# Kernel tuning notes

Measured on AMD Instinct MI355X. Metric: run time of the kernel, lower is better.

Reference implementation:

```python
import jax, jax.numpy as jnp
import numpy as np

N_NODES = 100000
N_EDGES = 600000
IN_FEAT = 128
OUT_FEAT = 128
NUM_RELS = 8
NUM_BASES = 4


def setup_inputs() -> dict:
    key = jax.random.key(0)
    ks = jax.random.split(key, 8)
    h = jax.random.normal(ks[0], (N_NODES, IN_FEAT), dtype=jnp.float32)
    # xavier-ish scale for params
    weight = jax.random.normal(ks[1], (NUM_BASES, IN_FEAT, OUT_FEAT), dtype=jnp.float32) * (1.0 / np.sqrt(IN_FEAT))
    w_comp = jax.random.normal(ks[2], (NUM_RELS, NUM_BASES), dtype=jnp.float32) * (1.0 / np.sqrt(NUM_BASES))
    root_weight = jax.random.normal(ks[3], (IN_FEAT, OUT_FEAT), dtype=jnp.float32) * (1.0 / np.sqrt(IN_FEAT))
    bias = jnp.zeros((OUT_FEAT,), dtype=jnp.float32)
    src = jax.random.randint(ks[4], (N_EDGES,), 0, N_NODES, dtype=jnp.int32)
    dst = jax.random.randint(ks[5], (N_EDGES,), 0, N_NODES, dtype=jnp.int32)
    rel_type = jax.random.randint(ks[6], (N_EDGES,), 0, NUM_RELS, dtype=jnp.int32)
    return {"h": h, "weight": weight, "w_comp": w_comp, "root_weight": root_weight,
            "bias": bias, "src": src, "dst": dst, "rel_type": rel_type}


def reference(h, weight, w_comp, root_weight, bias, src, dst, rel_type):
    # Basis decomposition: W[r] = sum_b w_comp[r,b] * weight[b]
    B, I, O = weight.shape
    R = w_comp.shape[0]
    W = (w_comp @ weight.reshape(B, I * O)).reshape(R, I, O)  # [R, in, out]
    # msg_e = h[src_e] @ W[rel_e]; computed as all-relation projection + gather
    # (avoids materializing [E, in, out] per-edge weights)
    proj = jnp.einsum('ni,rio->nro', h, W)          # [N, R, out]
    msg = proj[src, rel_type]                        # [E, out]
    agg = jax.ops.segment_sum(msg, dst, num_segments=h.shape[0])  # scatter-sum
    out = h @ root_weight + agg + bias
    return jax.nn.relu(out)
```

## Files before the change

kernel.cpp:

```cpp
#include <hip/hip_runtime.h>
#include <hip/hip_bf16.h>

#define N_NODES 100000
#define N_EDGES 600000
#define FEAT 128
#define NUM_RELS 8
#define NUM_BASES 4
#define NBE 2344

#define PREP_CAST 6250
#define PREP_BLDB 320
#define PREP_ZERO 392
#define PREP_GRID (PREP_CAST + PREP_BLDB + PREP_ZERO)

#define SCAN_TILES 98

typedef short bf16x8 __attribute__((ext_vector_type(8)));
typedef float f32x4  __attribute__((ext_vector_type(4)));
typedef float f32x2  __attribute__((ext_vector_type(2)));

__device__ inline short f2bf(float x) {
    __hip_bfloat16 b = __float2bfloat16(x);
    return *reinterpret_cast<short*>(&b);
}


__global__ __launch_bounds__(256) void k_prep(const float* __restrict__ h,
                                              const float* __restrict__ weight,
                                              const float* __restrict__ rw,
                                              short* __restrict__ hb,
                                              short* __restrict__ Btf,
                                              int* __restrict__ cnt,
                                              int* __restrict__ status) {
    int b = blockIdx.x;
    if (b < PREP_CAST) {
        int i = b * 256 + threadIdx.x;
        const float4* h4 = (const float4*)h;
        float4 v0 = h4[2 * i], v1 = h4[2 * i + 1];
        union { short s[8]; bf16x8 v; } u;
        u.s[0] = f2bf(v0.x); u.s[1] = f2bf(v0.y); u.s[2] = f2bf(v0.z); u.s[3] = f2bf(v0.w);
        u.s[4] = f2bf(v1.x); u.s[5] = f2bf(v1.y); u.s[6] = f2bf(v1.z); u.s[7] = f2bf(v1.w);
        ((bf16x8*)hb)[i] = u.v;
    } else if (b < PREP_CAST + PREP_BLDB) {
        int idx = (b - PREP_CAST) * 256 + threadIdx.x;
        int kc = idx >> 14;
        int e  = idx & 16383;
        int o  = e >> 7, ip = e & 127;
        float v = (kc == 0) ? rw[ip * FEAT + o]
                            : weight[(kc - 1) * FEAT * FEAT + ip * FEAT + o];
        int nt = o & 7, n16 = o >> 3;
        int ks = ip >> 5, quad = (ip >> 3) & 3, j = ip & 7;
        int lane = quad * 16 + n16;
        Btf[((kc * 4 + ks) * 8 + nt) * 512 + lane * 8 + j] = f2bf(v);
    } else {
        int i = (b - PREP_CAST - PREP_BLDB) * 256 + threadIdx.x;
        if (i < N_NODES) cnt[i] = 0;
        else if (i - N_NODES < 128) status[i - N_NODES] = 0;
    }
}

__global__ __launch_bounds__(256) void k_hist_dst(const int* __restrict__ dst,
                                                  int* __restrict__ cnt) {
    int i = blockIdx.x * 256 + threadIdx.x;
    if (i < N_EDGES) atomicAdd(&cnt[dst[i]], 1);
}

__global__ __launch_bounds__(256) void k_scan_lb(const int* __restrict__ cnt,
                                                 int* __restrict__ offs,
                                                 int* __restrict__ cursor,
                                                 int* __restrict__ status) {
    __shared__ int wsum[4];
    __shared__ int bcast;
    int bid = blockIdx.x;
    int lane = threadIdx.x & 63, wid = threadIdx.x >> 6;
    const int N4 = N_NODES / 4;
    int i4 = bid * 256 + threadIdx.x;

    const int4* cnt4 = (const int4*)cnt;
    int4 v = (i4 < N4) ? cnt4[i4] : make_int4(0, 0, 0, 0);
    int s = v.x + v.y + v.z + v.w;
    int incl = s;
#pragma unroll
    for (int d = 1; d < 64; d <<= 1) {
        int t = __shfl_up(incl, d);
        if (lane >= d) incl += t;
    }
    if (lane == 63) wsum[wid] = incl;
    __syncthreads();
    int total = wsum[0] + wsum[1] + wsum[2] + wsum[3];

    if (threadIdx.x < 64) {
        int excl = 0;
        if (bid > 0) {
            if (lane == 0)
                __hip_atomic_store(&status[bid], (total << 2) | 1,
                                   __ATOMIC_RELEASE, __HIP_MEMORY_SCOPE_AGENT);
            int winEnd = bid;
            for (;;) {
                int idx = winEnd - 64 + lane;
                int st = 2;
                if (idx >= 0) {
                    st = __hip_atomic_load(&status[idx],
                                           __ATOMIC_ACQUIRE, __HIP_MEMORY_SCOPE_AGENT);
                    while ((st & 3) == 0) {
                        __builtin_amdgcn_s_sleep(1);
                        st = __hip_atomic_load(&status[idx],
                                               __ATOMIC_ACQUIRE, __HIP_MEMORY_SCOPE_AGENT);
                    }
                }
                unsigned long long done = __ballot((st & 3) == 2);
                int contrib;
                if (done) {
                    int L = 63 - __builtin_clzll(done);
                    contrib = (lane >= L) ? (st >> 2) : 0;
                } else {
                    contrib = st >> 2;
                }
#pragma unroll
                for (int m = 1; m < 64; m <<= 1) contrib += __shfl_xor(contrib, m);
                excl += contrib;
                if (done) break;
                winEnd -= 64;
            }
        }
        if (lane == 0) {
            __hip_atomic_store(&status[bid], ((excl + total) << 2) | 2,
                               __ATOMIC_RELEASE, __HIP_MEMORY_SCOPE_AGENT);
            bcast = excl;
            if (bid == SCAN_TILES - 1) offs[N_NODES] = excl + total;
        }
    }
    __syncthreads();
    int wexcl = 0;
#pragma unroll
    for (int w = 0; w < 4; ++w) if (w < wid) wexcl += wsum[w];
    int base = bcast + wexcl + incl - s;
    if (i4 < N4) {
        int4 ex;
        ex.x = base;
        ex.y = base + v.x;
        ex.z = base + v.x + v.y;
        ex.w = base + v.x + v.y + v.z;
        ((int4*)offs)[i4]   = ex;
        ((int4*)cursor)[i4] = ex;
    }
}

__global__ __launch_bounds__(256) void k_scatter_sorted(const int* __restrict__ src,
                                                        const int* __restrict__ dst,
                                                        const int* __restrict__ rel,
                                                        int* __restrict__ cursor,
                                                        int* __restrict__ packed) {
    int e = blockIdx.x * 256 + threadIdx.x;
    if (e < N_EDGES) {
        int p = atomicAdd(&cursor[dst[e]], 1);
        packed[p] = (src[e] << 3) | rel[e];
    }
}

#define RL(pk, j) __builtin_amdgcn_readlane(pk, j)
#define EDGE_ACC(zz, c, v)                                               \
    {   f32x2 hh; hh.x = __int_as_float((v) << 16);                      \
        hh.y = __int_as_float((v) & 0xffff0000u);                        \
        f32x2 cc;                                                        \
        cc = c.x; zz[0] += cc * hh;                                      \
        cc = c.y; zz[1] += cc * hh;                                      \
        cc = c.z; zz[2] += cc * hh;                                      \
        cc = c.w; zz[3] += cc * hh; }

__global__ __launch_bounds__(256) void k_edge_z(const int* __restrict__ offs,
                                                const int* __restrict__ packed,
                                                const float* __restrict__ wc,
                                                const short* __restrict__ hb,
                                                unsigned int* __restrict__ z_u32) {
    int wid = threadIdx.x >> 6, lane = threadIdx.x & 63;
    int d0 = blockIdx.x * 8 + wid * 2;
    int s0 = offs[d0], sM = offs[d0 + 1], e1 = offs[d0 + 2];

    const float4* wc4 = (const float4*)wc;
    const unsigned int* hbu = (const unsigned int*)hb;

    f32x2 za[4] = {(f32x2)0.f, (f32x2)0.f, (f32x2)0.f, (f32x2)0.f};
    f32x2 zb[4] = {(f32x2)0.f, (f32x2)0.f, (f32x2)0.f, (f32x2)0.f};

    int baseA = s0, baseB = sM;
    while (baseA < sM || baseB < e1) {
        int mA = sM - baseA; mA = mA < 0 ? 0 : (mA > 64 ? 64 : mA);
        int mB = e1 - baseB; mB = mB < 0 ? 0 : (mB > 64 ? 64 : mB);
        int pkA = (lane < mA) ? packed[baseA + lane] : 0;
        int pkB = (lane < mB) ? packed[baseB + lane] : 0;
        int jA = 0, jB = 0;

        while (jA + 3 < mA && jB + 3 < mB) {
            int a0 = RL(pkA, jA), a1 = RL(pkA, jA + 1), a2 = RL(pkA, jA + 2), a3 = RL(pkA, jA + 3);
            int b0 = RL(pkB, jB), b1 = RL(pkB, jB + 1), b2 = RL(pkB, jB + 2), b3 = RL(pkB, jB + 3);
            unsigned int va0 = hbu[(size_t)(a0 >> 3) * 64 + lane];
            unsigned int va1 = hbu[(size_t)(a1 >> 3) * 64 + lane];
            unsigned int va2 = hbu[(size_t)(a2 >> 3) * 64 + lane];
            unsigned int va3 = hbu[(size_t)(a3 >> 3) * 64 + lane];
            unsigned int vb0 = hbu[(size_t)(b0 >> 3) * 64 + lane];
            unsigned int vb1 = hbu[(size_t)(b1 >> 3) * 64 + lane];
            unsigned int vb2 = hbu[(size_t)(b2 >> 3) * 64 + lane];
            unsigned int vb3 = hbu[(size_t)(b3 >> 3) * 64 + lane];
            float4 ca0 = wc4[a0 & 7], ca1 = wc4[a1 & 7], ca2 = wc4[a2 & 7], ca3 = wc4[a3 & 7];
            float4 cb0 = wc4[b0 & 7], cb1 = wc4[b1 & 7], cb2 = wc4[b2 & 7], cb3 = wc4[b3 & 7];
            EDGE_ACC(za, ca0, va0); EDGE_ACC(za, ca1, va1);
            EDGE_ACC(za, ca2, va2); EDGE_ACC(za, ca3, va3);
            EDGE_ACC(zb, cb0, vb0); EDGE_ACC(zb, cb1, vb1);
            EDGE_ACC(zb, cb2, vb2); EDGE_ACC(zb, cb3, vb3);
            jA += 4; jB += 4;
        }
        while (jA < mA && jB < mB) {
            int a0 = RL(pkA, jA), b0 = RL(pkB, jB);
            unsigned int va0 = hbu[(size_t)(a0 >> 3) * 64 + lane];
            unsigned int vb0 = hbu[(size_t)(b0 >> 3) * 64 + lane];
            float4 ca0 = wc4[a0 & 7], cb0 = wc4[b0 & 7];
            EDGE_ACC(za, ca0, va0);
            EDGE_ACC(zb, cb0, vb0);
            ++jA; ++jB;
        }
        while (jA + 3 < mA) {
            int a0 = RL(pkA, jA), a1 = RL(pkA, jA + 1), a2 = RL(pkA, jA + 2), a3 = RL(pkA, jA + 3);
            unsigned int va0 = hbu[(size_t)(a0 >> 3) * 64 + lane];
            unsigned int va1 = hbu[(size_t)(a1 >> 3) * 64 + lane];
            unsigned int va2 = hbu[(size_t)(a2 >> 3) * 64 + lane];
            unsigned int va3 = hbu[(size_t)(a3 >> 3) * 64 + lane];
            float4 ca0 = wc4[a0 & 7], ca1 = wc4[a1 & 7], ca2 = wc4[a2 & 7], ca3 = wc4[a3 & 7];
            EDGE_ACC(za, ca0, va0); EDGE_ACC(za, ca1, va1);
            EDGE_ACC(za, ca2, va2); EDGE_ACC(za, ca3, va3);
            jA += 4;
        }
        while (jA < mA) {
            int a0 = RL(pkA, jA);
            unsigned int va0 = hbu[(size_t)(a0 >> 3) * 64 + lane];
            float4 ca0 = wc4[a0 & 7];
            EDGE_ACC(za, ca0, va0);
            ++jA;
        }
        while (jB + 3 < mB) {
            int b0 = RL(pkB, jB), b1 = RL(pkB, jB + 1), b2 = RL(pkB, jB + 2), b3 = RL(pkB, jB + 3);
            unsigned int vb0 = hbu[(size_t)(b0 >> 3) * 64 + lane];
            unsigned int vb1 = hbu[(size_t)(b1 >> 3) * 64 + lane];
            unsigned int vb2 = hbu[(size_t)(b2 >> 3) * 64 + lane];
            unsigned int vb3 = hbu[(size_t)(b3 >> 3) * 64 + lane];
            float4 cb0 = wc4[b0 & 7], cb1 = wc4[b1 & 7], cb2 = wc4[b2 & 7], cb3 = wc4[b3 & 7];
            EDGE_ACC(zb, cb0, vb0); EDGE_ACC(zb, cb1, vb1);
            EDGE_ACC(zb, cb2, vb2); EDGE_ACC(zb, cb3, vb3);
            jB += 4;
        }
        while (jB < mB) {
            int b0 = RL(pkB, jB);
            unsigned int vb0 = hbu[(size_t)(b0 >> 3) * 64 + lane];
            float4 cb0 = wc4[b0 & 7];
            EDGE_ACC(zb, cb0, vb0);
            ++jB;
        }
        baseA += 64; baseB += 64;
    }

    unsigned int* row0 = z_u32 + (size_t)d0 * 256;
    unsigned int* row1 = row0 + 256;
#pragma unroll
    for (int b = 0; b < 4; ++b) {
        unsigned int lo0 = ((unsigned int)(unsigned short)f2bf(za[b].x));
        unsigned int hi0 = ((unsigned int)(unsigned short)f2bf(za[b].y)) << 16;
        row0[b * 64 + lane] = lo0 | hi0;
        unsigned int lo1 = ((unsigned int)(unsigned short)f2bf(zb[b].x));
        unsigned int hi1 = ((unsigned int)(unsigned short)f2bf(zb[b].y)) << 16;
        row1[b * 64 + lane] = lo1 | hi1;
    }
}

__global__ __launch_bounds__(256) void k_gemm_fused(const short* __restrict__ hb,
                                                    const short* __restrict__ z,
                                                    const short* __restrict__ Btf,
                                                    const float* __restrict__ bias,
                                                    float* __restrict__ out) {
    __shared__ short lds[FEAT * FEAT];
    int wave = threadIdx.x >> 6, lane = threadIdx.x & 63;
    int quad = lane >> 4, n16 = lane & 15;
    int base = blockIdx.x * 64 + wave * 16;

    int rowA = base + n16;
    if (rowA >= N_NODES) rowA = N_NODES - 1;

    f32x4 acc[8];
#pragma unroll
    for (int nt = 0; nt < 8; ++nt) acc[nt] = (f32x4)0.f;

    const bf16x8* bp = (const bf16x8*)lds;
    char* lds_base = (char*)lds;

    bf16x8 a_cur[4];
    {
        const bf16x8* ap = (const bf16x8*)(hb + (size_t)rowA * FEAT);
#pragma unroll
        for (int ks = 0; ks < 4; ++ks) a_cur[ks] = ap[ks * 4 + quad];
    }

    for (int kc = 0; kc < 5; ++kc) {
        if (kc) __syncthreads();
        const char* gsrc = (const char*)Btf + kc * 32768;
#pragma unroll
        for (int t = 0; t < 8; ++t) {
            unsigned int off = wave * 8192 + t * 1024;
            __builtin_amdgcn_global_load_lds(
                (const __attribute__((address_space(1))) unsigned int*)(gsrc + off + lane * 16),
                (__attribute__((address_space(3))) unsigned int*)(lds_base + off),
                16, 0, 0);
        }
        __syncthreads();

        bf16x8 a_nxt[4];
        if (kc < 4) {
            const bf16x8* ap = (const bf16x8*)(z + (size_t)rowA * 512 + kc * FEAT);
#pragma unroll
            for (int ks = 0; ks < 4; ++ks) a_nxt[ks] = ap[ks * 4 + quad];
        }

#pragma unroll
        for (int ks = 0; ks < 4; ++ks) {
            const bf16x8* bks = bp + ks * 512 + lane;
#pragma unroll
            for (int nt = 0; nt < 8; ++nt) {
                bf16x8 b = bks[nt * 64];
                acc[nt] = __builtin_amdgcn_mfma_f32_16x16x32_bf16(a_cur[ks], b, acc[nt], 0, 0, 0);
            }
        }

        if (kc < 4) {
#pragma unroll
            for (int ks = 0; ks < 4; ++ks) a_cur[ks] = a_nxt[ks];
        }
    }

    float bv[8];
#pragma unroll
    for (int nt = 0; nt < 8; ++nt) bv[nt] = bias[n16 * 8 + nt];

#pragma unroll
    for (int reg = 0; reg < 4; ++reg) {
        int node = base + quad * 4 + reg;
        if (node < N_NODES) {
            float4 fa, fb;
            fa.x = fmaxf(acc[0][reg] + bv[0], 0.f);
            fa.y = fmaxf(acc[1][reg] + bv[1], 0.f);
            fa.z = fmaxf(acc[2][reg] + bv[2], 0.f);
            fa.w = fmaxf(acc[3][reg] + bv[3], 0.f);
            fb.x = fmaxf(acc[4][reg] + bv[4], 0.f);
            fb.y = fmaxf(acc[5][reg] + bv[5], 0.f);
            fb.z = fmaxf(acc[6][reg] + bv[6], 0.f);
            fb.w = fmaxf(acc[7][reg] + bv[7], 0.f);
            float* row = out + (size_t)node * FEAT + n16 * 8;
            *(float4*)row       = fa;
            *(float4*)(row + 4) = fb;
        }
    }
}


extern "C" void kernel_launch(void* const* d_in, const int* in_sizes, int n_in,
                              void* d_out, int out_size, void* d_ws, size_t ws_size,
                              hipStream_t stream) {
    const float* h    = (const float*)d_in[0];
    const float* wgt  = (const float*)d_in[1];
    const float* wcmp = (const float*)d_in[2];
    const float* rw   = (const float*)d_in[3];
    const float* bias = (const float*)d_in[4];
    const int*   src  = (const int*)d_in[5];
    const int*   dst  = (const int*)d_in[6];
    const int*   rel  = (const int*)d_in[7];
    float* out = (float*)d_out;

    char* ws = (char*)d_ws;
    short*        hb     = (short*)(ws + 0);
    short*        Btf    = (short*)(ws + 25600000ull);
    short*        z      = (short*)(ws + 25763840ull);
    unsigned int* z_u32  = (unsigned int*)z;
    int*          packed = (int*)(ws + 128163840ull);
    int*          cnt    = (int*)(ws + 130563840ull);
    int*          offs   = (int*)(ws + 130963840ull);
    int*          cursor = (int*)(ws + 131363968ull);
    int*          status = (int*)(ws + 131763968ull);

    hipLaunchKernelGGL(k_prep,     dim3(PREP_GRID), dim3(256), 0, stream,
                       h, wgt, rw, hb, Btf, cnt, status);
    hipLaunchKernelGGL(k_hist_dst, dim3(NBE),  dim3(256), 0, stream, dst, cnt);
    hipLaunchKernelGGL(k_scan_lb,  dim3(SCAN_TILES), dim3(256), 0, stream,
                       cnt, offs, cursor, status);
    hipLaunchKernelGGL(k_scatter_sorted, dim3(NBE), dim3(256), 0, stream,
                       src, dst, rel, cursor, packed);
    hipLaunchKernelGGL(k_edge_z,   dim3(N_NODES / 8), dim3(256), 0, stream,
                       offs, packed, wcmp, hb, z_u32);
    hipLaunchKernelGGL(k_gemm_fused, dim3((N_NODES + 63) / 64), dim3(256), 0, stream,
                       hb, z, Btf, bias, out);
}
```

Baseline: 253.6 us.

## Hold fused GEMM weights in registers and split output columns across waves

The final fused GEMM no longer stages the 128x640 bf16 weight matrix through LDS. Each wave now keeps its own 32-column slice of B in registers for all K chunks and computes 16 rows. Each block covers 16 nodes instead of 64, so the grid grows fourfold. This removes the LDS staging loads and the __syncthreads barriers, but each block re-reads the whole weight matrix from global/L2, register pressure rises (160 VGPRs of B per lane), and every wave redundantly loads the same A rows.

Result: slower. 308.0 us (+21.5%).

```diff
diff --git a/kernel.cpp b/kernel.cpp
--- a/kernel.cpp
+++ b/kernel.cpp
@@ -271,25 +271,27 @@
     }
 }
 
-__global__ __launch_bounds__(256) void k_gemm_fused(const short* __restrict__ hb,
-                                                    const short* __restrict__ z,
-                                                    const short* __restrict__ Btf,
-                                                    const float* __restrict__ bias,
-                                                    float* __restrict__ out) {
-    __shared__ short lds[FEAT * FEAT];
+__global__ __launch_bounds__(256, 2) void k_gemm_reg(const short* __restrict__ hb,
+                                                     const short* __restrict__ z,
+                                                     const short* __restrict__ Btf,
+                                                     const float* __restrict__ bias,
+                                                     float* __restrict__ out) {
     int wave = threadIdx.x >> 6, lane = threadIdx.x & 63;
     int quad = lane >> 4, n16 = lane & 15;
-    int base = blockIdx.x * 64 + wave * 16;
-
+    int nq = wave;
+    int base = blockIdx.x * 16;
     int rowA = base + n16;
-    if (rowA >= N_NODES) rowA = N_NODES - 1;
-
-    f32x4 acc[8];
-#pragma unroll
-    for (int nt = 0; nt < 8; ++nt) acc[nt] = (f32x4)0.f;
-
-    const bf16x8* bp = (const bf16x8*)lds;
-    char* lds_base = (char*)lds;
+
+    const bf16x8* bf = (const bf16x8*)Btf;
+
+    bf16x8 B[5][4][2];
+#pragma unroll
+    for (int kc = 0; kc < 5; ++kc)
+#pragma unroll
+        for (int ks = 0; ks < 4; ++ks)
+#pragma unroll
+            for (int j = 0; j < 2; ++j)
+                B[kc][ks][j] = bf[((kc * 4 + ks) * 8 + nq * 2 + j) * 64 + lane];
 
     bf16x8 a_cur[4];
     {
@@ -298,63 +300,38 @@
         for (int ks = 0; ks < 4; ++ks) a_cur[ks] = ap[ks * 4 + quad];
     }
 
+    f32x4 acc[2];
+    acc[0] = (f32x4)0.f; acc[1] = (f32x4)0.f;
+
+#pragma unroll
     for (int kc = 0; kc < 5; ++kc) {
-        if (kc) __syncthreads();
-        const char* gsrc = (const char*)Btf + kc * 32768;
-#pragma unroll
-        for (int t = 0; t < 8; ++t) {
-            unsigned int off = wave * 8192 + t * 1024;
-            __builtin_amdgcn_global_load_lds(
-                (const __attribute__((address_space(1))) unsigned int*)(gsrc + off + lane * 16),
-                (__attribute__((address_space(3))) unsigned int*)(lds_base + off),
-                16, 0, 0);
-        }
-        __syncthreads();
-
         bf16x8 a_nxt[4];
         if (kc < 4) {
             const bf16x8* ap = (const bf16x8*)(z + (size_t)rowA * 512 + kc * FEAT);
 #pragma unroll
             for (int ks = 0; ks < 4; ++ks) a_nxt[ks] = ap[ks * 4 + quad];
         }
-
 #pragma unroll
         for (int ks = 0; ks < 4; ++ks) {
-            const bf16x8* bks = bp + ks * 512 + lane;
-#pragma unroll
-            for (int nt = 0; nt < 8; ++nt) {
-                bf16x8 b = bks[nt * 64];
-                acc[nt] = __builtin_amdgcn_mfma_f32_16x16x32_bf16(a_cur[ks], b, acc[nt], 0, 0, 0);
-            }
-        }
-
+            acc[0] = __builtin_amdgcn_mfma_f32_16x16x32_bf16(a_cur[ks], B[kc][ks][0], acc[0], 0, 0, 0);
+            acc[1] = __builtin_amdgcn_mfma_f32_16x16x32_bf16(a_cur[ks], B[kc][ks][1], acc[1], 0, 0, 0);
+        }
         if (kc < 4) {
 #pragma unroll
             for (int ks = 0; ks < 4; ++ks) a_cur[ks] = a_nxt[ks];
         }
     }
 
-    float bv[8];
-#pragma unroll
-    for (int nt = 0; nt < 8; ++nt) bv[nt] = bias[n16 * 8 + nt];
+    float bv0 = bias[n16 * 8 + nq * 2];
+    float bv1 = bias[n16 * 8 + nq * 2 + 1];
 
 #pragma unroll
     for (int reg = 0; reg < 4; ++reg) {
         int node = base + quad * 4 + reg;
-        if (node < N_NODES) {
-            float4 fa, fb;
-            fa.x = fmaxf(acc[0][reg] + bv[0], 0.f);
-            fa.y = fmaxf(acc[1][reg] + bv[1], 0.f);
-            fa.z = fmaxf(acc[2][reg] + bv[2], 0.f);
-            fa.w = fmaxf(acc[3][reg] + bv[3], 0.f);
-            fb.x = fmaxf(acc[4][reg] + bv[4], 0.f);
-            fb.y = fmaxf(acc[5][reg] + bv[5], 0.f);
-            fb.z = fmaxf(acc[6][reg] + bv[6], 0.f);
-            fb.w = fmaxf(acc[7][reg] + bv[7], 0.f);
-            float* row = out + (size_t)node * FEAT + n16 * 8;
-            *(float4*)row       = fa;
-            *(float4*)(row + 4) = fb;
-        }
+        float2 f;
+        f.x = fmaxf(acc[0][reg] + bv0, 0.f);
+        f.y = fmaxf(acc[1][reg] + bv1, 0.f);
+        *(float2*)(out + (size_t)node * FEAT + n16 * 8 + nq * 2) = f;
     }
 }
 
@@ -392,6 +369,6 @@
                        src, dst, rel, cursor, packed);
     hipLaunchKernelGGL(k_edge_z,   dim3(N_NODES / 8), dim3(256), 0, stream,
                        offs, packed, wcmp, hb, z_u32);
-    hipLaunchKernelGGL(k_gemm_fused, dim3((N_NODES + 63) / 64), dim3(256), 0, stream,
+    hipLaunchKernelGGL(k_gemm_reg, dim3(N_NODES / 16), dim3(256), 0, stream,
                        hb, z, Btf, bias, out);
 }
```
